# Performance work log

Measured on AMD Instinct MI355X. Metric: run time of the kernel, lower is better.

The kernel has to match this reference:

```python
import jax, jax.numpy as jnp
import numpy as np

D_MODEL = 2048
D_FF = 8192


def _act_quant(x):
    # BitNet b1.58 per-token int8 absmax activation quantization with STE passthrough
    scale = 127.0 / jnp.clip(jnp.max(jnp.abs(x), axis=-1, keepdims=True), 1e-5)
    xq = jnp.clip(jnp.round(x * scale), -128.0, 127.0) / scale
    return x + jax.lax.stop_gradient(xq - x)


def _weight_quant(w):
    # Ternary {-1,0,1} weight quantization with per-tensor mean-abs scale
    scale = 1.0 / jnp.clip(jnp.mean(jnp.abs(w)), 1e-5)
    wq = jnp.clip(jnp.round(w * scale), -1.0, 1.0) / scale
    return w + jax.lax.stop_gradient(wq - w)


def _bitlinear(x, w):
    # y = Q_act(x) @ Q_w(w)^T   (w has shape [out, in], torch Linear convention)
    return jnp.einsum('bsd,fd->bsf', _act_quant(x), _weight_quant(w))


def setup_inputs() -> dict:
    key = jax.random.key(0)
    k_x, k_w1, k_w2 = jax.random.split(key, 3)
    x = jax.random.normal(k_x, (4, 4096, D_MODEL), dtype=jnp.float32)
    # torch Linear default init scale ~ 1/sqrt(fan_in)
    W1 = jax.random.normal(k_w1, (D_FF, D_MODEL), dtype=jnp.float32) / np.sqrt(D_MODEL)
    W2 = jax.random.normal(k_w2, (D_MODEL, D_FF), dtype=jnp.float32) / np.sqrt(D_FF)
    return {"x": x, "W1": W1, "W2": W2}


def reference(x, W1, W2):
    h = jax.nn.silu(_bitlinear(x, W1))   # [B, S, d_ff]
    return _bitlinear(h, W2)             # [B, S, d_model]; dropout p=0 -> identity
```

## Files before the change

kernel.cpp:

```cpp
#include <hip/hip_runtime.h>
#include <hip/hip_bf16.h>
#include <cstdint>

#define DM 2048
#define DF 8192

typedef int v4i __attribute__((ext_vector_type(4)));
typedef int v16i __attribute__((ext_vector_type(16)));
typedef short v8s __attribute__((ext_vector_type(8)));

__device__ __forceinline__ float silu_f(float y) {
  return y * (1.0f / (1.0f + expf(-y)));
}

__device__ __forceinline__ void gload_lds16(const void* g, void* l) {
  __builtin_amdgcn_global_load_lds(
      (const __attribute__((address_space(1))) void*)g,
      (__attribute__((address_space(3))) void*)l, 16, 0, 0);
}

__global__ __launch_bounds__(256) void abs_sum_k(const float* __restrict__ w,
                                                 float* __restrict__ partial) {
  const int t = threadIdx.x;
  const float4* wp = (const float4*)w;
  const long base = (long)blockIdx.x * 4096;
  float s = 0.f;
#pragma unroll
  for (int i = 0; i < 16; ++i) {
    float4 v = wp[base + i * 256 + t];
    s += fabsf(v.x) + fabsf(v.y) + fabsf(v.z) + fabsf(v.w);
  }
#pragma unroll
  for (int d = 1; d < 64; d <<= 1) s += __shfl_xor(s, d, 64);
  __shared__ float wsum[4];
  if ((t & 63) == 0) wsum[t >> 6] = s;
  __syncthreads();
  if (t == 0) partial[blockIdx.x] = (wsum[0] + wsum[1]) + (wsum[2] + wsum[3]);
}

__global__ __launch_bounds__(256) void finalize_scales_k(const float* __restrict__ p1,
                                                         const float* __restrict__ p2,
                                                         float* __restrict__ sc) {
  const float* p = (blockIdx.x == 0) ? p1 : p2;
  const int t = threadIdx.x;
  float s = (p[t] + p[t + 256]) + (p[t + 512] + p[t + 768]);
#pragma unroll
  for (int d = 1; d < 64; d <<= 1) s += __shfl_xor(s, d, 64);
  __shared__ float wsum[4];
  if ((t & 63) == 0) wsum[t >> 6] = s;
  __syncthreads();
  if (t == 0) {
    float total = (wsum[0] + wsum[1]) + (wsum[2] + wsum[3]);
    float mean = total * (1.0f / 16777216.0f);
    float c = fmaxf(mean, 1e-5f);
    sc[blockIdx.x * 2 + 0] = 1.0f / c;
    sc[blockIdx.x * 2 + 1] = c;
  }
}

__global__ __launch_bounds__(256) void tern_quant_k(const float* __restrict__ w,
                                                    int8_t* __restrict__ wq,
                                                    const float* __restrict__ scp) {
  const float s = scp[0];
  const long i = (long)blockIdx.x * 256 + threadIdx.x;
  float4 v = ((const float4*)w)[i];
  int q0 = (int)rintf(v.x * s); q0 = q0 < -1 ? -1 : (q0 > 1 ? 1 : q0);
  int q1 = (int)rintf(v.y * s); q1 = q1 < -1 ? -1 : (q1 > 1 ? 1 : q1);
  int q2 = (int)rintf(v.z * s); q2 = q2 < -1 ? -1 : (q2 > 1 ? 1 : q2);
  int q3 = (int)rintf(v.w * s); q3 = q3 < -1 ? -1 : (q3 > 1 ? 1 : q3);
  ((int*)wq)[i] = (q0 & 255) | ((q1 & 255) << 8) | ((q2 & 255) << 16) | ((q3 & 255) << 24);
}

__global__ __launch_bounds__(256) void act_quant_x_k(const float* __restrict__ x,
                                                     int8_t* __restrict__ xq,
                                                     float* __restrict__ inv_sx) {
  const int t = threadIdx.x;
  const long row = blockIdx.x;
  const float4* xr = (const float4*)(x + row * DM);
  float4 v0 = xr[t * 2], v1 = xr[t * 2 + 1];
  float m = fmaxf(fmaxf(fmaxf(fabsf(v0.x), fabsf(v0.y)), fmaxf(fabsf(v0.z), fabsf(v0.w))),
                  fmaxf(fmaxf(fabsf(v1.x), fabsf(v1.y)), fmaxf(fabsf(v1.z), fabsf(v1.w))));
#pragma unroll
  for (int d = 1; d < 64; d <<= 1) m = fmaxf(m, __shfl_xor(m, d, 64));
  __shared__ float wm[4];
  if ((t & 63) == 0) wm[t >> 6] = m;
  __syncthreads();
  m = fmaxf(fmaxf(wm[0], wm[1]), fmaxf(wm[2], wm[3]));
  const float scale = 127.0f / fmaxf(m, 1e-5f);
  if (t == 0) inv_sx[row] = 1.0f / scale;
  float vv[8] = {v0.x, v0.y, v0.z, v0.w, v1.x, v1.y, v1.z, v1.w};
  int q[8];
#pragma unroll
  for (int j = 0; j < 8; ++j) {
    int qq = (int)rintf(vv[j] * scale);
    q[j] = qq < -128 ? -128 : (qq > 127 ? 127 : qq);
  }
  int lo = (q[0] & 255) | ((q[1] & 255) << 8) | ((q[2] & 255) << 16) | ((q[3] & 255) << 24);
  int hi = (q[4] & 255) | ((q[5] & 255) << 8) | ((q[6] & 255) << 16) | ((q[7] & 255) << 24);
  ((int2*)(xq + row * DM))[t] = make_int2(lo, hi);
}

__device__ __forceinline__ void stage_part(const int8_t* s, uint8_t* d, long Kl) {
  gload_lds16(s, d);
  gload_lds16(s + 32 * Kl, d + 4096);
  gload_lds16(s + 64 * Kl, d + 8192);
  gload_lds16(s + 96 * Kl, d + 12288);
}

__device__ __forceinline__ void rd_frags(const uint8_t* sA, const uint8_t* sB,
                                         int rowA, int cks,
                                         v4i (&Af)[4], v4i (&Bf)[4]) {
#pragma unroll
  for (int q = 0; q < 4; ++q) {
    Af[q] = *(const v4i*)(sA + q * 4096 + rowA + cks);
    Bf[q] = *(const v4i*)(sB + q * 4096 + rowA + cks);
  }
}

__device__ __forceinline__ void mfma16(const v4i (&Af)[4], const v4i (&Bf)[4],
                                       v16i (&acc)[4][4]) {
#pragma unroll
  for (int mt = 0; mt < 4; ++mt)
#pragma unroll
    for (int nt = 0; nt < 4; ++nt)
      acc[mt][nt] = __builtin_amdgcn_mfma_i32_32x32x32_i8(Af[mt], Bf[nt], acc[mt][nt], 0, 0, 0);
}

template <int K, int N, int EPI>
__global__ __launch_bounds__(256, 1) void gemm4_i8_k(
    const int8_t* __restrict__ A, const int8_t* __restrict__ B,
    const float* __restrict__ rowInv, const float* __restrict__ invswp,
    short* __restrict__ Y16, float* __restrict__ rowmaxP,
    float* __restrict__ Out) {
  constexpr int NT = K / 128;
  constexpr int NBX = N / 256;
  constexpr int NSTX = NBX / 4;
  __shared__ __align__(16) uint8_t lds[131072];

  const int t = threadIdx.x;
  const int wave = t >> 6;
  const int lane = t & 63;
  const int wr = wave >> 1, wc = wave & 1;
  const int l31 = lane & 31, kg = lane >> 5;

  const int cpx = (int)gridDim.x >> 3;
  const int bid0 = blockIdx.x;
  const int bid = (bid0 & 7) * cpx + (bid0 >> 3);
  const int st = bid >> 5, u = bid & 31;
  const int by = (st / NSTX) * 8 + (u >> 2);
  const int bx = (st % NSTX) * 4 + (u & 3);
  const long arow0 = (long)by * 256;
  const long bcol0 = (long)bx * 256;

  const int srow8 = t >> 3;
  const int scol = ((t & 7) ^ (srow8 & 7)) << 4;
  const int8_t* src0 = A + (arow0 + srow8) * (long)K + scol;
  const int8_t* src1 = src0 + (long)128 * K;
  const int8_t* src2 = B + (bcol0 + srow8) * (long)K + scol;
  const int8_t* src3 = src2 + (long)128 * K;
  uint8_t* dstb = lds + (wave << 10);

  const uint8_t* sAbase = lds + (wr << 14);
  const uint8_t* sBbase = lds + ((2 + wc) << 14);
  const int rowA = l31 * 128;
  const int swz = (l31 & 7) << 4;

  v16i acc[4][4] = {};
  v4i A0[4], B0[4], A1[4], B1[4];

#define STAGE_ALL(kk)                                                      \
  do {                                                                     \
    if ((kk) < NT) {                                                       \
      const long ko = (long)(kk) << 7;                                     \
      uint8_t* db = dstb + (((kk) & 1) << 16);                             \
      stage_part(src0 + ko, db, K);                                        \
      stage_part(src1 + ko, db + 16384, K);                                \
      stage_part(src2 + ko, db + 32768, K);                                \
      stage_part(src3 + ko, db + 49152, K);                                \
    }                                                                      \
  } while (0)

  STAGE_ALL(0);
  __syncthreads();

  for (int kt = 0; kt < NT; ++kt) {
    const uint8_t* sA = sAbase + ((kt & 1) << 16);
    const uint8_t* sB = sBbase + ((kt & 1) << 16);
    rd_frags(sA, sB, rowA, (0 * 32 + kg * 16) ^ swz, A0, B0);
    STAGE_ALL(kt + 1);
    rd_frags(sA, sB, rowA, (1 * 32 + kg * 16) ^ swz, A1, B1);
    mfma16(A0, B0, acc);
    rd_frags(sA, sB, rowA, (2 * 32 + kg * 16) ^ swz, A0, B0);
    mfma16(A1, B1, acc);
    rd_frags(sA, sB, rowA, (3 * 32 + kg * 16) ^ swz, A1, B1);
    mfma16(A0, B0, acc);
    mfma16(A1, B1, acc);
    __syncthreads();
  }

  const float invsw = invswp[0];
  if constexpr (EPI == 1) {
#pragma unroll
    for (int mt = 0; mt < 4; ++mt)
#pragma unroll
      for (int nt = 0; nt < 4; ++nt)
#pragma unroll
        for (int r = 0; r < 16; ++r) {
          const int row = wr * 128 + mt * 32 + (r & 3) + 8 * (r >> 2) + 4 * kg;
          const int col = wc * 128 + nt * 32 + l31;
          int yi = acc[mt][nt][r];
          int ys = yi < -32767 ? -32767 : (yi > 32767 ? 32767 : yi);
          *(short*)(lds + ((row * 512 + col * 2) ^ ((row & 7) << 4))) = (short)ys;
        }
    __syncthreads();
    const long grow = arow0 + t;
    const float c1v = rowInv[grow] * invsw;
    float mx = 0.f;
    short* gp = Y16 + grow * (long)DF + bcol0;
#pragma unroll
    for (int i = 0; i < 32; ++i) {
      v8s yv = *(const v8s*)(lds + ((t * 512 + i * 16) ^ ((t & 7) << 4)));
#pragma unroll
      for (int j = 0; j < 8; ++j) mx = fmaxf(mx, fabsf(silu_f((float)yv[j] * c1v)));
      *(v8s*)(gp + i * 8) = yv;
    }
    rowmaxP[grow * NBX + bx] = mx;
  } else {
#pragma unroll
    for (int mt = 0; mt < 4; ++mt)
#pragma unroll
      for (int r = 0; r < 16; ++r) {
        const long grow = arow0 + wr * 128 + mt * 32 + (r & 3) + 8 * (r >> 2) + 4 * kg;
        const float c2 = rowInv[grow] * invsw;
#pragma unroll
        for (int nt = 0; nt < 4; ++nt)
          Out[grow * N + bcol0 + wc * 128 + nt * 32 + l31] = (float)acc[mt][nt][r] * c2;
      }
  }
#undef STAGE_ALL
}

__global__ __launch_bounds__(256) void quant_h_k(const short* __restrict__ Y16,
                                                 const float* __restrict__ rowmaxP,
                                                 const float* __restrict__ inv_sx,
                                                 const float* __restrict__ sc,
                                                 int8_t* __restrict__ hq,
                                                 float* __restrict__ inv_sh) {
  const int t = threadIdx.x;
  const long row = blockIdx.x;
  __shared__ float smax_s;
  if (t < 64) {
    float m = (t < 32) ? rowmaxP[row * 32 + t] : 0.f;
#pragma unroll
    for (int d = 1; d < 64; d <<= 1) m = fmaxf(m, __shfl_xor(m, d, 64));
    if (t == 0) smax_s = m;
  }
  __syncthreads();
  const float scale = 127.0f / fmaxf(smax_s, 1e-5f);
  if (t == 0) inv_sh[row] = 1.0f / scale;
  const float c1 = inv_sx[row] * sc[1];
  const short4* yp = (const short4*)(Y16 + row * DF);
  int* op = (int*)(hq + row * DF);
#pragma unroll
  for (int b = 0; b < 8; ++b) {
    short4 s4 = yp[b * 256 + t];
    short vals[4] = {s4.x, s4.y, s4.z, s4.w};
    int q[4];
#pragma unroll
    for (int j = 0; j < 4; ++j) {
      float h = silu_f((float)vals[j] * c1);
      int qq = (int)rintf(h * scale);
      q[j] = qq < -128 ? -128 : (qq > 127 ? 127 : qq);
    }
    op[b * 256 + t] = (q[0] & 255) | ((q[1] & 255) << 8) | ((q[2] & 255) << 16) | ((q[3] & 255) << 24);
  }
}

extern "C" void kernel_launch(void* const* d_in, const int* in_sizes, int n_in,
                              void* d_out, int out_size, void* d_ws, size_t ws_size,
                              hipStream_t stream) {
  const float* x = (const float*)d_in[0];
  const float* W1 = (const float*)d_in[1];
  const float* W2 = (const float*)d_in[2];
  float* out = (float*)d_out;

  uint8_t* w = (uint8_t*)d_ws;
  float* sc = (float*)(w + 0);
  float* p1 = (float*)(w + 256);
  float* p2 = (float*)(w + 256 + 4096);
  float* inv_sx = (float*)(w + 8448);
  float* inv_sh = (float*)(w + 8448 + 65536);
  float* rowmaxP = (float*)(w + 8448 + 131072);
  uint8_t* w1q = w + 8448 + 131072 + 4194304;
  uint8_t* w2q = w1q + 16777216;
  uint8_t* xq = w2q + 16777216;
  uint8_t* hq = xq + 33554432;
  short* y16 = (short*)(hq + 134217728);

  abs_sum_k<<<1024, 256, 0, stream>>>(W1, p1);
  abs_sum_k<<<1024, 256, 0, stream>>>(W2, p2);
  finalize_scales_k<<<2, 256, 0, stream>>>(p1, p2, sc);
  tern_quant_k<<<16384, 256, 0, stream>>>(W1, (int8_t*)w1q, sc + 0);
  tern_quant_k<<<16384, 256, 0, stream>>>(W2, (int8_t*)w2q, sc + 2);
  act_quant_x_k<<<16384, 256, 0, stream>>>(x, (int8_t*)xq, inv_sx);
  gemm4_i8_k<2048, 8192, 1><<<2048, 256, 0, stream>>>(
      (const int8_t*)xq, (const int8_t*)w1q, inv_sx, sc + 1, y16, rowmaxP, nullptr);
  quant_h_k<<<16384, 256, 0, stream>>>(y16, rowmaxP, inv_sx, sc, (int8_t*)hq, inv_sh);
  gemm4_i8_k<8192, 2048, 0><<<512, 256, 0, stream>>>(
      (const int8_t*)hq, (const int8_t*)w2q, inv_sh, sc + 3, nullptr, nullptr, out);
}
```

Measured before the change: 889.6 us.

## Remap LDS staging layout and interleave MFMA with loads via sched_group_barrier

Changes how the int8 GEMM stages tiles into LDS: each wave now loads a different row/column pattern with a new XOR swizzle, and fragment reads use matching row bases and precomputed column offsets. It adds sched_group_barrier hints so LDS reads, global-to-LDS loads and MFMAs interleave in a fixed order inside each k-step, aiming to hide memory latency behind matrix math. The h quantization kernel is also widened to 16-byte loads and 8-byte stores. The forced schedule could raise register pressure or stall if the hint groups do not match the actual instruction counts.

```diff
diff --git a/kernel.cpp b/kernel.cpp
--- a/kernel.cpp
+++ b/kernel.cpp
@@ -100,20 +100,13 @@
   ((int2*)(xq + row * DM))[t] = make_int2(lo, hi);
 }
 
-__device__ __forceinline__ void stage_part(const int8_t* s, uint8_t* d, long Kl) {
-  gload_lds16(s, d);
-  gload_lds16(s + 32 * Kl, d + 4096);
-  gload_lds16(s + 64 * Kl, d + 8192);
-  gload_lds16(s + 96 * Kl, d + 12288);
-}
-
-__device__ __forceinline__ void rd_frags(const uint8_t* sA, const uint8_t* sB,
-                                         int rowA, int cks,
-                                         v4i (&Af)[4], v4i (&Bf)[4]) {
+__device__ __forceinline__ void rdset(const uint8_t* Ap, const uint8_t* Bp,
+                                      int rbase, int cks,
+                                      v4i (&Af)[4], v4i (&Bf)[4]) {
 #pragma unroll
   for (int q = 0; q < 4; ++q) {
-    Af[q] = *(const v4i*)(sA + q * 4096 + rowA + cks);
-    Bf[q] = *(const v4i*)(sB + q * 4096 + rowA + cks);
+    Af[q] = *(const v4i*)(Ap + q * 4096 + rbase + cks);
+    Bf[q] = *(const v4i*)(Bp + q * 4096 + rbase + cks);
   }
 }
 
@@ -152,49 +145,69 @@
   const long arow0 = (long)by * 256;
   const long bcol0 = (long)bx * 256;
 
-  const int srow8 = t >> 3;
-  const int scol = ((t & 7) ^ (srow8 & 7)) << 4;
-  const int8_t* src0 = A + (arow0 + srow8) * (long)K + scol;
-  const int8_t* src1 = src0 + (long)128 * K;
-  const int8_t* src2 = B + (bcol0 + srow8) * (long)K + scol;
-  const int8_t* src3 = src2 + (long)128 * K;
-  uint8_t* dstb = lds + (wave << 10);
-
-  const uint8_t* sAbase = lds + (wr << 14);
-  const uint8_t* sBbase = lds + ((2 + wc) << 14);
-  const int rowA = l31 * 128;
-  const int swz = (l31 & 7) << 4;
+  const int s_r15 = wave * 4 + (lane >> 4);
+  const int s_row = s_r15 + 16 * ((lane >> 3) & 1);
+  const int s_j = (lane & 7) ^ (s_r15 & 7);
+  const long stg_off = (long)s_row * K + (s_j << 4);
+
+  const int8_t* psrc0 = A + arow0 * K;
+  const int8_t* psrc1 = psrc0 + (long)128 * K;
+  const int8_t* psrc2 = B + bcol0 * K;
+  const int8_t* psrc3 = psrc2 + (long)128 * K;
+
+  const int rbase = (lane & 15) * 256 + ((lane >> 4) & 1) * 128;
+  const int c0 = ((0 | kg) ^ (lane & 7)) << 4;
+  const int c1 = ((2 | kg) ^ (lane & 7)) << 4;
+  const int c2 = ((4 | kg) ^ (lane & 7)) << 4;
+  const int c3 = ((6 | kg) ^ (lane & 7)) << 4;
 
   v16i acc[4][4] = {};
-  v4i A0[4], B0[4], A1[4], B1[4];
-
-#define STAGE_ALL(kk)                                                      \
+  v4i SA0[4], SB0[4], SA1[4], SB1[4];
+
+#define STAGEP(kk_, part_, ps_)                                            \
   do {                                                                     \
-    if ((kk) < NT) {                                                       \
-      const long ko = (long)(kk) << 7;                                     \
-      uint8_t* db = dstb + (((kk) & 1) << 16);                             \
-      stage_part(src0 + ko, db, K);                                        \
-      stage_part(src1 + ko, db + 16384, K);                                \
-      stage_part(src2 + ko, db + 32768, K);                                \
-      stage_part(src3 + ko, db + 49152, K);                                \
+    if ((kk_) < NT) {                                                      \
+      uint8_t* d = lds + (((kk_) & 1) << 16) + ((part_) << 14) + (wave << 10); \
+      const int8_t* s = (ps_) + (((long)(kk_)) << 7) + stg_off;            \
+      gload_lds16(s, d);                                                   \
+      gload_lds16(s + 32 * (long)K, d + 4096);                             \
+      gload_lds16(s + 64 * (long)K, d + 8192);                             \
+      gload_lds16(s + 96 * (long)K, d + 12288);                            \
     }                                                                      \
   } while (0)
 
-  STAGE_ALL(0);
+#define SGB(m_, n_) __builtin_amdgcn_sched_group_barrier((m_), (n_), 0)
+
+  STAGEP(0, 0, psrc0); STAGEP(0, 1, psrc1);
+  STAGEP(0, 2, psrc2); STAGEP(0, 3, psrc3);
   __syncthreads();
 
   for (int kt = 0; kt < NT; ++kt) {
-    const uint8_t* sA = sAbase + ((kt & 1) << 16);
-    const uint8_t* sB = sBbase + ((kt & 1) << 16);
-    rd_frags(sA, sB, rowA, (0 * 32 + kg * 16) ^ swz, A0, B0);
-    STAGE_ALL(kt + 1);
-    rd_frags(sA, sB, rowA, (1 * 32 + kg * 16) ^ swz, A1, B1);
-    mfma16(A0, B0, acc);
-    rd_frags(sA, sB, rowA, (2 * 32 + kg * 16) ^ swz, A0, B0);
-    mfma16(A1, B1, acc);
-    rd_frags(sA, sB, rowA, (3 * 32 + kg * 16) ^ swz, A1, B1);
-    mfma16(A0, B0, acc);
-    mfma16(A1, B1, acc);
+    const uint8_t* Ap = lds + ((kt & 1) << 16) + (wr << 14);
+    const uint8_t* Bp = lds + ((kt & 1) << 16) + ((2 + wc) << 14);
+
+    rdset(Ap, Bp, rbase, c0, SA0, SB0);
+    STAGEP(kt + 1, 0, psrc0);
+    STAGEP(kt + 1, 1, psrc1);
+    STAGEP(kt + 1, 2, psrc2);
+    STAGEP(kt + 1, 3, psrc3);
+    rdset(Ap, Bp, rbase, c1, SA1, SB1);
+    mfma16(SA0, SB0, acc);
+    rdset(Ap, Bp, rbase, c2, SA0, SB0);
+    mfma16(SA1, SB1, acc);
+    rdset(Ap, Bp, rbase, c3, SA1, SB1);
+    mfma16(SA0, SB0, acc);
+    mfma16(SA1, SB1, acc);
+
+    SGB(0x100, 8);
+    SGB(0x20, 16);
+    SGB(0x100, 2); SGB(8, 4); SGB(0x100, 2); SGB(8, 4);
+    SGB(0x100, 2); SGB(8, 4); SGB(0x100, 2); SGB(8, 4);
+    SGB(0x100, 2); SGB(8, 4); SGB(0x100, 2); SGB(8, 4);
+    SGB(0x100, 2); SGB(8, 4); SGB(0x100, 2); SGB(8, 4);
+    SGB(0x100, 2); SGB(8, 4); SGB(0x100, 2); SGB(8, 4);
+    SGB(0x100, 2); SGB(8, 4); SGB(0x100, 2); SGB(8, 4);
+    SGB(8, 16);
     __syncthreads();
   }
 
@@ -231,13 +244,14 @@
 #pragma unroll
       for (int r = 0; r < 16; ++r) {
         const long grow = arow0 + wr * 128 + mt * 32 + (r & 3) + 8 * (r >> 2) + 4 * kg;
-        const float c2 = rowInv[grow] * invsw;
+        const float cc = rowInv[grow] * invsw;
 #pragma unroll
         for (int nt = 0; nt < 4; ++nt)
-          Out[grow * N + bcol0 + wc * 128 + nt * 32 + l31] = (float)acc[mt][nt][r] * c2;
+          Out[grow * N + bcol0 + wc * 128 + nt * 32 + l31] = (float)acc[mt][nt][r] * cc;
       }
   }
-#undef STAGE_ALL
+#undef STAGEP
+#undef SGB
 }
 
 __global__ __launch_bounds__(256) void quant_h_k(const short* __restrict__ Y16,
@@ -259,20 +273,21 @@
   const float scale = 127.0f / fmaxf(smax_s, 1e-5f);
   if (t == 0) inv_sh[row] = 1.0f / scale;
   const float c1 = inv_sx[row] * sc[1];
-  const short4* yp = (const short4*)(Y16 + row * DF);
-  int* op = (int*)(hq + row * DF);
-#pragma unroll
-  for (int b = 0; b < 8; ++b) {
-    short4 s4 = yp[b * 256 + t];
-    short vals[4] = {s4.x, s4.y, s4.z, s4.w};
-    int q[4];
-#pragma unroll
-    for (int j = 0; j < 4; ++j) {
-      float h = silu_f((float)vals[j] * c1);
+  const v8s* yp = (const v8s*)(Y16 + row * DF);
+  int2* op = (int2*)(hq + row * DF);
+#pragma unroll
+  for (int b = 0; b < 4; ++b) {
+    v8s s8 = yp[b * 256 + t];
+    int q[8];
+#pragma unroll
+    for (int j = 0; j < 8; ++j) {
+      float h = silu_f((float)s8[j] * c1);
       int qq = (int)rintf(h * scale);
       q[j] = qq < -128 ? -128 : (qq > 127 ? 127 : qq);
     }
-    op[b * 256 + t] = (q[0] & 255) | ((q[1] & 255) << 8) | ((q[2] & 255) << 16) | ((q[3] & 255) << 24);
+    int lo = (q[0] & 255) | ((q[1] & 255) << 8) | ((q[2] & 255) << 16) | ((q[3] & 255) << 24);
+    int hi = (q[4] & 255) | ((q[5] & 255) << 8) | ((q[6] & 255) << 16) | ((q[7] & 255) << 24);
+    op[b * 256 + t] = make_int2(lo, hi);
   }
 }
 
```

Result: no change. 890.2 us (+0.1%).
